# Kernel tuning notes

Measured on AMD Instinct MI355X. Metric: run time of the kernel, lower is better.

## Reference

```python
import jax, jax.numpy as jnp
import numpy as np
from jax import lax

# pywt Wavelet('db3') analysis filters (dec_lo, dec_hi)
DEC_LO = jnp.array([0.035226291882100656, -0.08544127388224149, -0.13501102001039084,
                    0.4598775021193313, 0.8068915093133388, 0.3326705529509569], dtype=jnp.float32)
DEC_HI = jnp.array([-0.3326705529509569, 0.8068915093133388, -0.4598775021193313,
                    -0.13501102001039084, 0.08544127388224149, 0.035226291882100656], dtype=jnp.float32)


def _dwt_level(x):
    # One analysis level of pytorch_wavelets DWT1D with mode='zero'.
    # x: [B, N] -> (lo, hi) each [B, (N+L-1)//2]
    N = x.shape[-1]
    L = DEC_LO.shape[0]
    outsize = (N + L - 1) // 2  # pywt.dwt_coeff_len, zero mode
    p = 2 * (outsize - 1) - N + L
    # conv_general_dilated does cross-correlation; reversed filter == true convolution
    w = jnp.stack([DEC_LO[::-1], DEC_HI[::-1]])[:, None, :]  # [2, 1, L]
    y = lax.conv_general_dilated(x[:, None, :], w, window_strides=(2,),
                                 padding=[(p // 2, p - p // 2)])  # [B, 2, outsize]
    return y[:, 0, :], y[:, 1, :]


def _wavelet_features(sig, level=3):
    # sig: [B, N]. Returns (mean of final low-pass, sum over levels of ||hf||_2) per row.
    lo = sig
    high = jnp.zeros(sig.shape[0], sig.dtype)
    for _ in range(level):
        lo, hi = _dwt_level(lo)
        high = high + jnp.sqrt(jnp.sum(hi * hi, axis=-1))
    return jnp.mean(lo, axis=-1), high


def _dirichlet_weight(low, high):
    # Deterministic surrogate: Dirichlet([a1*10, a2*10]) has mean a1/(a1+a2),
    # replacing scipy dirichlet.rvs sampling with its expectation.
    a1 = jnp.clip(low, 1e-6)
    a2 = jnp.clip(high, 1e-6)
    return a1 / (a1 + a2)


def _forward(user_idx, item_idx, values, num_users, num_items):
    # item popularity: scatter-add of values * log1p(interaction count), L2-normalized
    counts = jnp.zeros(num_items, jnp.float32).at[item_idx].add(1.0)
    log_counts = jnp.log1p(counts)
    pop = jnp.zeros(num_items, jnp.float32).at[item_idx].add(values * log_counts[item_idx])
    pop = pop / (jnp.linalg.norm(pop) + 1e-8)
    # user activity
    act = jnp.zeros(num_users, jnp.float32).at[user_idx].add(
        values / jnp.log1p(pop[item_idx] + 1e-8))
    act = act / (jnp.linalg.norm(act) + 1e-8)
    # dense per-entity interaction signals (batched scatter replaces per-entity masking loop)
    user_sig = jnp.zeros((num_users, num_items), jnp.float32).at[user_idx, item_idx].add(values)
    user_sig = user_sig * (1.0 + act)[:, None]
    item_sig = jnp.zeros((num_items, num_users), jnp.float32).at[item_idx, user_idx].add(values)
    item_sig = item_sig * (1.0 + pop)[:, None]
    u_low, u_high = _wavelet_features(user_sig)
    i_low, i_high = _wavelet_features(item_sig)
    u_pop = _dirichlet_weight(u_low, u_high)
    i_pop = _dirichlet_weight(i_low, i_high)
    u_ni, i_ni = 1.0 - u_pop, 1.0 - i_pop
    wu_p, wu_n = u_pop[user_idx], u_ni[user_idx]
    wi_p, wi_n = i_pop[item_idx], i_ni[item_idx]
    # nnz-valued sparse outputs: [UIPG(=pop/pop), UING(=niche/niche), pop/niche, niche/pop]
    return jnp.stack([values * wu_p * wi_p,
                      values * wu_n * wi_n,
                      values * wu_p * wi_n,
                      values * wu_n * wi_p])


def setup_inputs():
    key = jax.random.key(0)
    k1, k2, k3 = jax.random.split(key, 3)
    NNZ, U, I = 2_000_000, 8192, 8192
    return {
        "user_idx": jax.random.randint(k1, (NNZ,), 0, U, dtype=jnp.int32),
        "item_idx": jax.random.randint(k2, (NNZ,), 0, I, dtype=jnp.int32),
        "values": jax.random.uniform(k3, (NNZ,), dtype=jnp.float32),
        "num_users": U,
        "num_items": I,
    }


def reference(user_idx, item_idx, values, num_users, num_items):
    return _forward(user_idx, item_idx, values, num_users, num_items)
```

## Files before the change

### kernel.cpp

```cpp
#include <hip/hip_runtime.h>
#include <math.h>

#define NE 8192
#define HT 1024
#define NCH 8
#define RT 512
#define NROWS 16

__device__ __constant__ float LO_R[6] = {
    0.3326705529509569f, 0.8068915093133388f, 0.4598775021193313f,
    -0.13501102001039084f, -0.08544127388224149f, 0.035226291882100656f};
__device__ __constant__ float HI_RV[6] = {
    0.035226291882100656f, 0.08544127388224149f, -0.13501102001039084f,
    -0.4598775021193313f, 0.8068915093133388f, -0.3326705529509569f};

__device__ __forceinline__ float blockReduceSum(float v, float* red) {
    #pragma unroll
    for (int off = 32; off > 0; off >>= 1) v += __shfl_down(v, off);
    int lane = threadIdx.x & 63, wid = threadIdx.x >> 6;
    if (lane == 0) red[wid] = v;
    __syncthreads();
    float r = 0.f;
    if (threadIdx.x == 0) {
        int nw = blockDim.x >> 6;
        for (int i = 0; i < nw; ++i) r += red[i];
    }
    return r;
}

__global__ void k_tables(float* __restrict__ resp, float4* __restrict__ Tdiag) {
    int a = blockIdx.x * blockDim.x + threadIdx.x;
    if (a >= NE) return;
    float lo1r[8], hi1r[8];
    int k1a = max(0, (a >> 1) - 3);
    #pragma unroll
    for (int t = 0; t < 8; ++t) {
        int k = k1a + t;
        int j = a - 2 * k + 4;
        bool ok = (j >= 0 && j <= 5 && k <= 4097);
        lo1r[t] = ok ? LO_R[j] : 0.f;
        hi1r[t] = ok ? HI_RV[j] : 0.f;
    }
    float lo2r[8], hi2r[8];
    int k2a = max(0, (k1a >> 1) - 1);
    #pragma unroll
    for (int t = 0; t < 8; ++t) {
        int k = k2a + t;
        float aL = 0.f, aH = 0.f;
        if (k <= 2050) {
            #pragma unroll
            for (int j = 0; j < 6; ++j) {
                int idx = 2 * k - 4 + j - k1a;
                if (idx >= 0 && idx < 8) {
                    aL = fmaf(LO_R[j], lo1r[idx], aL);
                    aH = fmaf(HI_RV[j], lo1r[idx], aH);
                }
            }
        }
        lo2r[t] = aL; hi2r[t] = aH;
    }
    float lo3r[8], hi3r[8];
    int k3a = max(0, (k2a >> 1) - 1);
    #pragma unroll
    for (int t = 0; t < 8; ++t) {
        int k = k3a + t;
        float aL = 0.f, aH = 0.f;
        if (k <= 1027) {
            #pragma unroll
            for (int j = 0; j < 6; ++j) {
                int idx = 2 * k - 4 + j - k2a;
                if (idx >= 0 && idx < 8) {
                    aL = fmaf(LO_R[j], lo2r[idx], aL);
                    aH = fmaf(HI_RV[j], lo2r[idx], aH);
                }
            }
        }
        lo3r[t] = aL; hi3r[t] = aH;
    }
    float g1 = 0.f, g2 = 0.f, g3 = 0.f, w3 = 0.f;
    #pragma unroll
    for (int t = 0; t < 8; ++t) {
        g1 = fmaf(hi1r[t], hi1r[t], g1);
        g2 = fmaf(hi2r[t], hi2r[t], g2);
        g3 = fmaf(hi3r[t], hi3r[t], g3);
        w3 += lo3r[t];
    }
    Tdiag[a] = make_float4(w3, g1, g2, g3);
    float* rp = resp + (size_t)a * 32;
    #pragma unroll
    for (int t = 0; t < 8; ++t) { rp[t] = hi1r[t]; rp[8 + t] = hi2r[t]; rp[16 + t] = hi3r[t]; }
    rp[24] = __int_as_float(k1a);
    rp[25] = __int_as_float(k2a);
    rp[26] = __int_as_float(k3a);
}

__global__ void k_gram(const float* __restrict__ resp, float* __restrict__ GtP) {
    int idx = blockIdx.x * 256 + threadIdx.x;
    if (idx >= NE * 35) return;
    int a = idx / 35;
    int d = idx - a * 35 + 1;
    int b = a + d;
    float v1 = 0.f, v2 = 0.f, v3 = 0.f;
    const float* ra = resp + (size_t)a * 32;
    if (b < NE) {
        const float* rb = resp + (size_t)b * 32;
        {
            int s = __float_as_int(rb[26]) - __float_as_int(ra[26]);
            #pragma unroll
            for (int u = 0; u < 8; ++u) {
                int t = u + s;
                if (t >= 0 && t < 8) v3 = fmaf(rb[16 + u], ra[16 + t], v3);
            }
        }
        if (d <= 15) {
            int s = __float_as_int(rb[25]) - __float_as_int(ra[25]);
            #pragma unroll
            for (int u = 0; u < 8; ++u) {
                int t = u + s;
                if (t >= 0 && t < 8) v2 = fmaf(rb[8 + u], ra[8 + t], v2);
            }
        }
        if (d <= 5) {
            int s = __float_as_int(rb[24]) - __float_as_int(ra[24]);
            #pragma unroll
            for (int u = 0; u < 8; ++u) {
                int t = u + s;
                if (t >= 0 && t < 8) v1 = fmaf(rb[u], ra[t], v1);
            }
        }
    }
    float* g = GtP + (size_t)a * 60;
    if (d <= 5) {
        *(float4*)(g + 4 * (d - 1)) = make_float4(v1, v2, v3, 0.f);
    } else if (d <= 15) {
        *(float2*)(g + 20 + 2 * (d - 6)) = make_float2(v2, v3);
    } else {
        g[40 + (d - 16)] = v3;
    }
}

__global__ __launch_bounds__(HT) void k_hist3(const int* __restrict__ ui,
                                              const int* __restrict__ ii,
                                              const float* __restrict__ v, int nnz,
                                              int* __restrict__ sliceU,
                                              int* __restrict__ sliceI,
                                              float* __restrict__ sliceS) {
    __shared__ int hU[NE];
    __shared__ int hI[NE];
    __shared__ float hS[NE];
    int b = blockIdx.x, tid = threadIdx.x, hb = gridDim.x;
    int4* hU4 = (int4*)hU; int4* hI4 = (int4*)hI; int4* hS4 = (int4*)hS;
    int4 z4 = make_int4(0, 0, 0, 0);
    for (int j = tid; j < NE / 4; j += HT) { hU4[j] = z4; hI4[j] = z4; hS4[j] = z4; }
    __syncthreads();
    int C = (nnz + hb - 1) / hb;
    int beg = b * C, end = min(nnz, beg + C);
    for (int n = beg + tid; n < end; n += HT) {
        atomicAdd(&hU[ui[n]], 1);
        int it = ii[n];
        atomicAdd(&hI[it], 1);
        atomicAdd(&hS[it], v[n]);
    }
    __syncthreads();
    size_t base = (size_t)b * NE;
    int4* sU = (int4*)(sliceU + base); int4* sI = (int4*)(sliceI + base);
    int4* sS = (int4*)(sliceS + base);
    for (int j = tid; j < NE / 4; j += HT) { sU[j] = hU4[j]; sI[j] = hI4[j]; sS[j] = hS4[j]; }
}

__global__ void k_chunksum3(const int* __restrict__ sliceU, const int* __restrict__ sliceI,
                            const float* __restrict__ sliceS, int spc,
                            int* __restrict__ csU, int* __restrict__ csI,
                            float* __restrict__ csS) {
    int i = blockIdx.x * 256 + threadIdx.x;
    int c = blockIdx.y;
    int b0 = c * spc;
    int cu = 0, ci = 0; float sv = 0.f;
    for (int b = b0; b < b0 + spc; ++b) {
        size_t o = (size_t)b * NE + i;
        cu += sliceU[o]; ci += sliceI[o]; sv += sliceS[o];
    }
    size_t oc = (size_t)c * NE + i;
    csU[oc] = cu; csI[oc] = ci; csS[oc] = sv;
}

__global__ void k_final3(const int* __restrict__ csU, const int* __restrict__ csI,
                         const float* __restrict__ csS,
                         int* cntU, int* cntI, float* popraw, float* normAcc) {
    __shared__ float red[4];
    int i = blockIdx.x * 256 + threadIdx.x;
    int cu = 0, ci = 0; float sv = 0.f;
    #pragma unroll
    for (int c = 0; c < NCH; ++c) {
        size_t o = (size_t)c * NE + i;
        cu += csU[o]; ci += csI[o]; sv += csS[o];
    }
    cntU[i] = cu; cntI[i] = ci;
    float p = log1pf((float)ci) * sv;
    popraw[i] = p;
    float s = blockReduceSum(p * p, red);
    if (threadIdx.x == 0) atomicAdd(&normAcc[0], s);
}

__global__ void k_scan2(const int* __restrict__ cntU, const int* __restrict__ cntI,
                        int* ptrU, int* ptrI) {
    __shared__ int sums[256];
    const int* cnt = blockIdx.x ? cntI : cntU;
    int* ptr = blockIdx.x ? ptrI : ptrU;
    int tid = threadIdx.x;
    int base = tid * 32;
    int local[32];
    int s = 0;
    #pragma unroll
    for (int j = 0; j < 32; ++j) { local[j] = cnt[base + j]; s += local[j]; }
    sums[tid] = s;
    __syncthreads();
    for (int off = 1; off < 256; off <<= 1) {
        int t = (tid >= off) ? sums[tid - off] : 0;
        __syncthreads();
        sums[tid] += t;
        __syncthreads();
    }
    int run = (tid > 0) ? sums[tid - 1] : 0;
    #pragma unroll
    for (int j = 0; j < 32; ++j) { ptr[base + j] = run; run += local[j]; }
    if (tid == 255) ptr[NE] = run;
}

__global__ void k_colscanB(int* csU, int* csI,
                           const int* __restrict__ ptrU, const int* __restrict__ ptrI) {
    int i = blockIdx.x * 256 + threadIdx.x;
    int* cs = blockIdx.y ? csI : csU;
    const int* ptr = blockIdx.y ? ptrI : ptrU;
    int run = ptr[i];
    #pragma unroll
    for (int c = 0; c < NCH; ++c) {
        size_t o = (size_t)c * NE + i;
        int t = cs[o]; cs[o] = run; run += t;
    }
}

__global__ void k_colscanC(int* sliceU, int* sliceI,
                           const int* __restrict__ csU, const int* __restrict__ csI, int spc) {
    int i = blockIdx.x * 256 + threadIdx.x;
    int c = blockIdx.y;
    int* slice = blockIdx.z ? sliceI : sliceU;
    const int* cs = blockIdx.z ? csI : csU;
    int run = cs[(size_t)c * NE + i];
    int b0 = c * spc;
    for (int b = b0; b < b0 + spc; ++b) {
        size_t o = (size_t)b * NE + i;
        int t = slice[o]; slice[o] = run; run += t;
    }
}

__global__ __launch_bounds__(HT) void k_scatter2(const int* __restrict__ ui,
                                                 const int* __restrict__ ii,
                                                 const float* __restrict__ v, int nnz,
                                                 const int* __restrict__ sliceU,
                                                 const int* __restrict__ sliceI,
                                                 const float* __restrict__ popraw,
                                                 const float* __restrict__ normAcc,
                                                 int2* __restrict__ pairsU,
                                                 int2* __restrict__ pairsI,
                                                 float* __restrict__ sliceA) {
    __shared__ int curU[NE];
    __shared__ int curI[NE];
    __shared__ float hA[NE];
    int b = blockIdx.x, tid = threadIdx.x, hb = gridDim.x;
    const int4* sU = (const int4*)(sliceU + (size_t)b * NE);
    const int4* sI = (const int4*)(sliceI + (size_t)b * NE);
    int4* cU4 = (int4*)curU; int4* cI4 = (int4*)curI;
    float4* hA4 = (float4*)hA;
    float4 zf = make_float4(0.f, 0.f, 0.f, 0.f);
    for (int j = tid; j < NE / 4; j += HT) { cU4[j] = sU[j]; cI4[j] = sI[j]; hA4[j] = zf; }
    __syncthreads();
    float rs0 = 1.f / (sqrtf(normAcc[0]) + 1e-8f);
    int C = (nnz + hb - 1) / hb;
    int beg = b * C, end = min(nnz, beg + C);
    for (int n = beg + tid; n < end; n += HT) {
        int u = ui[n], it = ii[n];
        float val = v[n];
        atomicAdd(&hA[u], val / log1pf(popraw[it] * rs0 + 1e-8f));
        int pU = atomicAdd(&curU[u], 1);
        pairsU[pU] = make_int2(it, __float_as_int(val));
        int pI = atomicAdd(&curI[it], 1);
        pairsI[pI] = make_int2(u, __float_as_int(val));
    }
    __syncthreads();
    float4* sA = (float4*)(sliceA + (size_t)b * NE);
    for (int j = tid; j < NE / 4; j += HT) sA[j] = hA4[j];
}

__global__ void k_actchunk(const float* __restrict__ sliceA, int spc, float* __restrict__ csA) {
    int i = blockIdx.x * 256 + threadIdx.x;
    int c = blockIdx.y;
    int b0 = c * spc;
    float a = 0.f;
    for (int b = b0; b < b0 + spc; ++b) a += sliceA[(size_t)b * NE + i];
    csA[(size_t)c * NE + i] = a;
}

__global__ void k_actfinal(const float* __restrict__ csA, float* act, float* normAcc) {
    __shared__ float red[4];
    int i = blockIdx.x * 256 + threadIdx.x;
    float a = 0.f;
    #pragma unroll
    for (int c = 0; c < NCH; ++c) a += csA[(size_t)c * NE + i];
    act[i] = a;
    float s = blockReduceSum(a * a, red);
    if (threadIdx.x == 0) atomicAdd(&normAcc[1], s);
}

__device__ __forceinline__ void scan_one(int p, float v, float4 td,
                                         const float* __restrict__ X,
                                         const unsigned int* __restrict__ Mrow,
                                         const float* __restrict__ GtP,
                                         float& s1, float& s2, float& s3, float& ls) {
    float xp = X[p];
    ls = fmaf(v, td.x, ls);
    float vx = v * xp;
    s1 = fmaf(vx, td.y, s1);
    s2 = fmaf(vx, td.z, s2);
    s3 = fmaf(vx, td.w, s3);
    int w = p >> 5, sh = (p & 31) + 1;
    unsigned long long lo64 = (unsigned long long)Mrow[w] |
                              ((unsigned long long)Mrow[w + 1] << 32);
    unsigned long long win = (lo64 >> sh) |
                             ((unsigned long long)Mrow[w + 2] << (64 - sh));
    win &= (1ull << 35) - 1ull;
    const float* g = GtP + (size_t)p * 60;
    while (win) {
        int d = __ffsll((unsigned long long)win);
        win &= win - 1;
        float c = 2.f * v * X[p + d];
        if (d <= 5) {
            float4 G = *(const float4*)(g + 4 * (d - 1));
            s1 = fmaf(c, G.x, s1);
            s2 = fmaf(c, G.y, s2);
            s3 = fmaf(c, G.z, s3);
        } else if (d <= 15) {
            float2 G = *(const float2*)(g + 20 + 2 * (d - 6));
            s2 = fmaf(c, G.x, s2);
            s3 = fmaf(c, G.y, s3);
        } else {
            s3 = fmaf(c, g[40 + (d - 16)], s3);
        }
    }
}

__global__ __launch_bounds__(RT) void k_rows(const int* __restrict__ ptrU,
                                             const int* __restrict__ ptrI,
                                             const int2* __restrict__ pairsU,
                                             const int2* __restrict__ pairsI,
                                             const float* __restrict__ popraw,
                                             const float* __restrict__ actraw,
                                             const float* __restrict__ normAcc,
                                             const float4* __restrict__ Tdiag,
                                             const float* __restrict__ GtP,
                                             float* __restrict__ u_w,
                                             float* __restrict__ i_w) {
    __shared__ __align__(16) float X[NE];
    __shared__ unsigned int M[264];
    __shared__ float acc[NROWS][4];
    int tid = threadIdx.x;
    int bid = blockIdx.x;
    bool isUser = bid >= 512;
    int r0 = (isUser ? bid - 512 : bid) * NROWS;
    const int* ptr = isUser ? ptrU : ptrI;
    const int2* pairs = isUser ? pairsU : pairsI;
    const float* raw = isUser ? actraw : popraw;
    float* w_out = isUser ? u_w : i_w;
    float rs = 1.f / (sqrtf(normAcc[isUser ? 1 : 0]) + 1e-8f);

    float4* X4 = (float4*)X;
    const float4 z4 = make_float4(0.f, 0.f, 0.f, 0.f);
    for (int q = tid; q < NE / 4; q += RT) X4[q] = z4;
    if (tid < 264) M[tid] = 0u;
    if (tid < NROWS * 4) ((float*)acc)[tid] = 0.f;

    int beg = ptr[r0], end = ptr[r0 + 1];
    int2 pr = make_int2(0, 0);
    float4 td = z4;
    if (tid < end - beg) {
        pr = pairs[beg + tid];
        td = Tdiag[pr.x];
    }

    for (int j = 0; j < NROWS; ++j) {
        int rl = r0 + j;
        __syncthreads();

        int cnt = end - beg;
        if (tid < cnt) {
            int p = pr.x;
            atomicAdd(&X[p], __int_as_float(pr.y));
            atomicOr(&M[p >> 5], 1u << (p & 31));
        }
        for (int n = beg + RT + tid; n < end; n += RT) {
            int2 q2 = pairs[n];
            atomicAdd(&X[q2.x], __int_as_float(q2.y));
            atomicOr(&M[q2.x >> 5], 1u << (q2.x & 31));
        }
        __syncthreads();

        int begN = end, endN = end;
        int2 prN = make_int2(0, 0);
        float4 tdN = z4;
        if (j + 1 < NROWS) {
            endN = ptr[rl + 2];
            if (tid < endN - begN) {
                prN = pairs[begN + tid];
                tdN = Tdiag[prN.x];
            }
        }

        float s1 = 0.f, s2 = 0.f, s3 = 0.f, ls = 0.f;
        if (tid < cnt)
            scan_one(pr.x, __int_as_float(pr.y), td, X, M, GtP, s1, s2, s3, ls);
        for (int n = beg + RT + tid; n < end; n += RT) {
            int2 q2 = pairs[n];
            scan_one(q2.x, __int_as_float(q2.y), Tdiag[q2.x], X, M, GtP,
                     s1, s2, s3, ls);
        }

        #pragma unroll
        for (int off = 32; off > 0; off >>= 1) {
            s1 += __shfl_down(s1, off);
            s2 += __shfl_down(s2, off);
            s3 += __shfl_down(s3, off);
            ls += __shfl_down(ls, off);
        }
        if ((tid & 63) == 0) {
            atomicAdd(&acc[j][0], s1);
            atomicAdd(&acc[j][1], s2);
            atomicAdd(&acc[j][2], s3);
            atomicAdd(&acc[j][3], ls);
        }
        __syncthreads();

        if (tid < cnt) { X[pr.x] = 0.f; M[pr.x >> 5] = 0u; }
        for (int n = beg + RT + tid; n < end; n += RT) {
            int2 q2 = pairs[n];
            X[q2.x] = 0.f; M[q2.x >> 5] = 0u;
        }
        beg = begN; end = endN; pr = prN; td = tdN;
    }

    __syncthreads();
    if (tid < NROWS) {
        float t1 = acc[tid][0], t2 = acc[tid][1], t3 = acc[tid][2], tl = acc[tid][3];
        float rawv = raw[r0 + tid];
        float sc = 1.f + rawv * rs;
        float high = (sqrtf(fmaxf(t1, 0.f)) + sqrtf(fmaxf(t2, 0.f)) +
                      sqrtf(fmaxf(t3, 0.f))) * sc;
        float low = tl * (1.f / 1028.f) * sc;
        float a1 = fmaxf(low, 1e-6f);
        float a2 = fmaxf(high, 1e-6f);
        w_out[r0 + tid] = a1 / (a1 + a2);
    }
}

__global__ void k_out(const int* __restrict__ ui, const int* __restrict__ ii,
                      const float* __restrict__ v, int nnz,
                      const float* __restrict__ u_w, const float* __restrict__ i_w,
                      float* __restrict__ out) {
    int ngroups = nnz >> 2;
    int idx = blockIdx.x * blockDim.x + threadIdx.x;
    int stride = gridDim.x * blockDim.x;
    const int4* ui4 = (const int4*)ui;
    const int4* ii4 = (const int4*)ii;
    const float4* v4 = (const float4*)v;
    float4* o0 = (float4*)out;
    float4* o1 = (float4*)(out + (size_t)nnz);
    float4* o2 = (float4*)(out + 2 * (size_t)nnz);
    float4* o3 = (float4*)(out + 3 * (size_t)nnz);
    for (int g = idx; g < ngroups; g += stride) {
        int4 u = ui4[g];
        int4 it = ii4[g];
        float4 val = v4[g];
        float wu0 = u_w[u.x], wu1 = u_w[u.y], wu2 = u_w[u.z], wu3 = u_w[u.w];
        float wi0 = i_w[it.x], wi1 = i_w[it.y], wi2 = i_w[it.z], wi3 = i_w[it.w];
        o0[g] = make_float4(val.x * wu0 * wi0, val.y * wu1 * wi1,
                            val.z * wu2 * wi2, val.w * wu3 * wi3);
        o1[g] = make_float4(val.x * (1.f - wu0) * (1.f - wi0), val.y * (1.f - wu1) * (1.f - wi1),
                            val.z * (1.f - wu2) * (1.f - wi2), val.w * (1.f - wu3) * (1.f - wi3));
        o2[g] = make_float4(val.x * wu0 * (1.f - wi0), val.y * wu1 * (1.f - wi1),
                            val.z * wu2 * (1.f - wi2), val.w * wu3 * (1.f - wi3));
        o3[g] = make_float4(val.x * (1.f - wu0) * wi0, val.y * (1.f - wu1) * wi1,
                            val.z * (1.f - wu2) * wi2, val.w * (1.f - wu3) * wi3);
    }
    int tail = ngroups * 4;
    for (int n = tail + idx; n < nnz; n += stride) {
        float val = v[n];
        float wu = u_w[ui[n]], wi = i_w[ii[n]];
        out[n] = val * wu * wi;
        out[(size_t)nnz + n] = val * (1.f - wu) * (1.f - wi);
        out[2 * (size_t)nnz + n] = val * wu * (1.f - wi);
        out[3 * (size_t)nnz + n] = val * (1.f - wu) * wi;
    }
}

extern "C" void kernel_launch(void* const* d_in, const int* in_sizes, int n_in,
                              void* d_out, int out_size, void* d_ws, size_t ws_size,
                              hipStream_t stream) {
    const int* ui = (const int*)d_in[0];
    const int* ii = (const int*)d_in[1];
    const float* vals = (const float*)d_in[2];
    int nnz = in_sizes[0];
    float* out = (float*)d_out;

    char* ws = (char*)d_ws;
    size_t off = 0;
    auto take = [&](size_t bytes) -> char* {
        char* p = ws + off;
        off = (off + bytes + 255) & ~(size_t)255;
        return p;
    };

    int*   cntU    = (int*)take(NE * 4);
    int*   cntI    = (int*)take(NE * 4);
    float* popraw  = (float*)take(NE * 4);
    float* actraw  = (float*)take(NE * 4);
    int*   ptrU    = (int*)take((NE + 1) * 4);
    int*   ptrI    = (int*)take((NE + 1) * 4);
    float* u_w     = (float*)take(NE * 4);
    float* i_w     = (float*)take(NE * 4);
    float* normAcc = (float*)take(256);
    float4* Tdiag  = (float4*)take((size_t)NE * 16);
    float* GtP     = (float*)take((size_t)NE * 60 * 4);
    float* resp    = (float*)take((size_t)NE * 32 * 4);
    int*   csU     = (int*)take((size_t)NCH * NE * 4);
    int*   csI     = (int*)take((size_t)NCH * NE * 4);
    float* csS     = (float*)take((size_t)NCH * NE * 4);
    int2*  pairsU  = (int2*)take((size_t)nnz * 8);
    int2*  pairsI  = (int2*)take((size_t)nnz * 8);
    size_t fixedEnd = off;

    int hb = 256;
    while (hb > 8 && fixedEnd + 3 * (size_t)hb * NE * 4 + 4096 > ws_size) hb >>= 1;
    int spc = hb / NCH;
    int*   sliceU = (int*)take((size_t)hb * NE * 4);
    int*   sliceI = (int*)take((size_t)hb * NE * 4);
    float* sliceS = (float*)take((size_t)hb * NE * 4);

    hipMemsetAsync(normAcc, 0, 256, stream);

    int nb = (nnz / 4 + 255) / 256;
    if (nb > 2048) nb = 2048;

    k_tables<<<NE / 64, 64, 0, stream>>>(resp, Tdiag);
    k_gram<<<(NE * 35 + 255) / 256, 256, 0, stream>>>(resp, GtP);

    k_hist3<<<hb, HT, 0, stream>>>(ui, ii, vals, nnz, sliceU, sliceI, sliceS);
    k_chunksum3<<<dim3(32, NCH), 256, 0, stream>>>(sliceU, sliceI, sliceS, spc, csU, csI, csS);
    k_final3<<<32, 256, 0, stream>>>(csU, csI, csS, cntU, cntI, popraw, normAcc);

    k_scan2<<<2, 256, 0, stream>>>(cntU, cntI, ptrU, ptrI);
    k_colscanB<<<dim3(32, 2), 256, 0, stream>>>(csU, csI, ptrU, ptrI);
    k_colscanC<<<dim3(32, NCH, 2), 256, 0, stream>>>(sliceU, sliceI, csU, csI, spc);

    k_scatter2<<<hb, HT, 0, stream>>>(ui, ii, vals, nnz, sliceU, sliceI,
                                      popraw, normAcc, pairsU, pairsI, sliceS);

    k_actchunk<<<dim3(32, NCH), 256, 0, stream>>>(sliceS, spc, csS);
    k_actfinal<<<32, 256, 0, stream>>>(csS, actraw, normAcc);

    k_rows<<<1024, RT, 0, stream>>>(ptrU, ptrI, pairsU, pairsI,
                                    popraw, actraw, normAcc, Tdiag, GtP, u_w, i_w);

    k_out<<<nb, 256, 0, stream>>>(ui, ii, vals, nnz, u_w, i_w, out);
}
```

Baseline: 243.9 us.

## Scatter with quarter as many blocks using coarsened scan offsets

The column-scan kernel now writes exclusive offsets only for every fourth histogram slice into a new compact scat buffer, instead of rewriting every slice in place. The scatter kernel runs with a quarter as many blocks, each covering four histogram chunks, so less per-block offset and activity-slice data is loaded and written. In k_rows, idle waves that hold no pairs now skip the shuffle reduction. The cost is more elements per scatter block and less parallelism, plus extra workspace for the scat buffers.

```diff
diff --git a/kernel.cpp b/kernel.cpp
--- a/kernel.cpp
+++ b/kernel.cpp
@@ -240,44 +240,46 @@
     }
 }
 
-__global__ void k_colscanC(int* sliceU, int* sliceI,
-                           const int* __restrict__ csU, const int* __restrict__ csI, int spc) {
+__global__ void k_colscanC(const int* __restrict__ sliceU, const int* __restrict__ sliceI,
+                           const int* __restrict__ csU, const int* __restrict__ csI,
+                           int* __restrict__ scatU, int* __restrict__ scatI, int spc) {
     int i = blockIdx.x * 256 + threadIdx.x;
     int c = blockIdx.y;
-    int* slice = blockIdx.z ? sliceI : sliceU;
+    const int* slice = blockIdx.z ? sliceI : sliceU;
     const int* cs = blockIdx.z ? csI : csU;
+    int* scat = blockIdx.z ? scatI : scatU;
     int run = cs[(size_t)c * NE + i];
     int b0 = c * spc;
     for (int b = b0; b < b0 + spc; ++b) {
-        size_t o = (size_t)b * NE + i;
-        int t = slice[o]; slice[o] = run; run += t;
+        if ((b & 3) == 0) scat[(size_t)(b >> 2) * NE + i] = run;
+        run += slice[(size_t)b * NE + i];
     }
 }
 
 __global__ __launch_bounds__(HT) void k_scatter2(const int* __restrict__ ui,
                                                  const int* __restrict__ ii,
                                                  const float* __restrict__ v, int nnz,
-                                                 const int* __restrict__ sliceU,
-                                                 const int* __restrict__ sliceI,
+                                                 const int* __restrict__ scatU,
+                                                 const int* __restrict__ scatI,
                                                  const float* __restrict__ popraw,
                                                  const float* __restrict__ normAcc,
                                                  int2* __restrict__ pairsU,
                                                  int2* __restrict__ pairsI,
-                                                 float* __restrict__ sliceA) {
+                                                 float* __restrict__ sliceA,
+                                                 int C256) {
     __shared__ int curU[NE];
     __shared__ int curI[NE];
     __shared__ float hA[NE];
-    int b = blockIdx.x, tid = threadIdx.x, hb = gridDim.x;
-    const int4* sU = (const int4*)(sliceU + (size_t)b * NE);
-    const int4* sI = (const int4*)(sliceI + (size_t)b * NE);
+    int b = blockIdx.x, tid = threadIdx.x;
+    const int4* sU = (const int4*)(scatU + (size_t)b * NE);
+    const int4* sI = (const int4*)(scatI + (size_t)b * NE);
     int4* cU4 = (int4*)curU; int4* cI4 = (int4*)curI;
     float4* hA4 = (float4*)hA;
     float4 zf = make_float4(0.f, 0.f, 0.f, 0.f);
     for (int j = tid; j < NE / 4; j += HT) { cU4[j] = sU[j]; cI4[j] = sI[j]; hA4[j] = zf; }
     __syncthreads();
     float rs0 = 1.f / (sqrtf(normAcc[0]) + 1e-8f);
-    int C = (nnz + hb - 1) / hb;
-    int beg = b * C, end = min(nnz, beg + C);
+    int beg = b * 4 * C256, end = min(nnz, beg + 4 * C256);
     for (int n = beg + tid; n < end; n += HT) {
         int u = ui[n], it = ii[n];
         float val = v[n];
@@ -424,18 +426,21 @@
                      s1, s2, s3, ls);
         }
 
-        #pragma unroll
-        for (int off = 32; off > 0; off >>= 1) {
-            s1 += __shfl_down(s1, off);
-            s2 += __shfl_down(s2, off);
-            s3 += __shfl_down(s3, off);
-            ls += __shfl_down(ls, off);
-        }
-        if ((tid & 63) == 0) {
-            atomicAdd(&acc[j][0], s1);
-            atomicAdd(&acc[j][1], s2);
-            atomicAdd(&acc[j][2], s3);
-            atomicAdd(&acc[j][3], ls);
+        int nwav = min(8, (cnt + 63) >> 6);
+        if ((tid >> 6) < nwav) {
+            #pragma unroll
+            for (int off = 32; off > 0; off >>= 1) {
+                s1 += __shfl_down(s1, off);
+                s2 += __shfl_down(s2, off);
+                s3 += __shfl_down(s3, off);
+                ls += __shfl_down(ls, off);
+            }
+            if ((tid & 63) == 0) {
+                atomicAdd(&acc[j][0], s1);
+                atomicAdd(&acc[j][1], s2);
+                atomicAdd(&acc[j][2], s3);
+                atomicAdd(&acc[j][3], ls);
+            }
         }
         __syncthreads();
 
@@ -538,16 +543,22 @@
     size_t fixedEnd = off;
 
     int hb = 256;
-    while (hb > 8 && fixedEnd + 3 * (size_t)hb * NE * 4 + 4096 > ws_size) hb >>= 1;
+    while (hb > 32 && fixedEnd + 3 * (size_t)hb * NE * 4 +
+                      2 * (size_t)(hb / 4) * NE * 4 + 4096 > ws_size) hb >>= 1;
+    int SCB = hb / 4;
     int spc = hb / NCH;
+    int spcA = SCB / NCH;
     int*   sliceU = (int*)take((size_t)hb * NE * 4);
     int*   sliceI = (int*)take((size_t)hb * NE * 4);
     float* sliceS = (float*)take((size_t)hb * NE * 4);
+    int*   scatU  = (int*)take((size_t)SCB * NE * 4);
+    int*   scatI  = (int*)take((size_t)SCB * NE * 4);
 
     hipMemsetAsync(normAcc, 0, 256, stream);
 
     int nb = (nnz / 4 + 255) / 256;
     if (nb > 2048) nb = 2048;
+    int C256 = (nnz + hb - 1) / hb;
 
     k_tables<<<NE / 64, 64, 0, stream>>>(resp, Tdiag);
     k_gram<<<(NE * 35 + 255) / 256, 256, 0, stream>>>(resp, GtP);
@@ -558,12 +569,13 @@
 
     k_scan2<<<2, 256, 0, stream>>>(cntU, cntI, ptrU, ptrI);
     k_colscanB<<<dim3(32, 2), 256, 0, stream>>>(csU, csI, ptrU, ptrI);
-    k_colscanC<<<dim3(32, NCH, 2), 256, 0, stream>>>(sliceU, sliceI, csU, csI, spc);
-
-    k_scatter2<<<hb, HT, 0, stream>>>(ui, ii, vals, nnz, sliceU, sliceI,
-                                      popraw, normAcc, pairsU, pairsI, sliceS);
-
-    k_actchunk<<<dim3(32, NCH), 256, 0, stream>>>(sliceS, spc, csS);
+    k_colscanC<<<dim3(32, NCH, 2), 256, 0, stream>>>(sliceU, sliceI, csU, csI,
+                                                     scatU, scatI, spc);
+
+    k_scatter2<<<SCB, HT, 0, stream>>>(ui, ii, vals, nnz, scatU, scatI,
+                                       popraw, normAcc, pairsU, pairsI, sliceS, C256);
+
+    k_actchunk<<<dim3(32, NCH), 256, 0, stream>>>(sliceS, spcA, csS);
     k_actfinal<<<32, 256, 0, stream>>>(csS, actraw, normAcc);
 
     k_rows<<<1024, RT, 0, stream>>>(ptrU, ptrI, pairsU, pairsI,
```

Result: slower. 277.8 us (+13.9%).
